# Optimization experiments

Measured on AMD Instinct MI355X. Metric: run time of the kernel, lower is better.

Reference implementation:

```python
import jax, jax.numpy as jnp
import numpy as np

B, N, T, D, DG, DS, NC = 16, 64, 256, 64, 64, 9, 2

def _pe(times, d, max_len):
    # PositionalEncodingTF: timescales = max_len ** linspace(0,1,d//2)
    ts = jnp.asarray(max_len ** np.linspace(0.0, 1.0, d // 2), jnp.float32)
    st = times[..., None] / ts
    return jnp.concatenate([jnp.sin(st), jnp.cos(st)], -1)

def _ln(h, g, b):
    m = h.mean(-1, keepdims=True)
    v = ((h - m) ** 2).mean(-1, keepdims=True)
    return (h - m) * jax.lax.rsqrt(v + 1e-5) * g + b

def setup_inputs():
    key = jax.random.key(0)
    ks = jax.random.split(key, 40)
    s = 0.02
    value = jax.random.normal(ks[0], (B, T, N))
    obs = (jax.random.uniform(ks[1], (B, T, N)) < 0.5).astype(jnp.float32)
    times = jnp.sort(jax.random.uniform(ks[2], (B, T)) * T, axis=1)
    F = D + 2 * DG  # per-node GRU input feature size [x_t, h, time_enc]
    return dict(
        x=jnp.concatenate([value, obs, times[..., None]], -1),
        nufft=jax.random.normal(ks[3], (B, 2, T, N)),
        delta_t=jax.random.uniform(ks[4], (B, T)) * 0.1,
        static=jax.random.normal(ks[5], (B, DS)),
        lengths=jax.random.randint(ks[6], (B,), 1, T + 1),
        proj_w=jax.random.normal(ks[7], (2, D)) * s, proj_b=jnp.zeros(D),
        Wqkv=jax.random.normal(ks[8], (D, 3 * D)) * s, bqkv=jnp.zeros(3 * D),
        Wo=jax.random.normal(ks[9], (D, D)) * s, bo=jnp.zeros(D),
        ln1_g=jnp.ones(D), ln1_b=jnp.zeros(D),
        W1=jax.random.normal(ks[10], (D, D)) * s, b1=jnp.zeros(D),
        W2=jax.random.normal(ks[11], (D, D)) * s, b2=jnp.zeros(D),
        ln2_g=jnp.ones(D), ln2_b=jnp.zeros(D),
        WQ_f=jax.random.normal(ks[12], (T, T)) * 0.05,
        WK_f=jax.random.normal(ks[13], (T, T)) * 0.05,
        Wz=jax.random.normal(ks[14], (2 * F, DG)) * s, bz=jnp.zeros(DG),
        Wr=jax.random.normal(ks[15], (2 * F, DG)) * s, br=jnp.zeros(DG),
        Wc=jax.random.normal(ks[16], (2 * F, DG)) * s, bc=jnp.zeros(DG),
        Wfin=jax.random.normal(ks[17], (DG,)) * s, bfin=jnp.zeros(()),
        We=jax.random.normal(ks[18], (DS, N)) * s, be=jnp.zeros(N),
        Wc1=jax.random.normal(ks[19], (2 * N, 200)) * s, bc1=jnp.zeros(200),
        Wc2=jax.random.normal(ks[20], (200, NC)) * s, bc2=jnp.zeros(NC),
    )

def _forward(x, nufft, delta_t, static, lengths, proj_w, proj_b, Wqkv, bqkv, Wo, bo,
             ln1_g, ln1_b, W1, b1, W2, b2, ln2_g, ln2_b, WQ_f, WK_f,
             Wz, bz, Wr, br, Wc, bc, Wfin, bfin, We, be, Wc1, bc1, Wc2, bc2):
    lengths = jnp.maximum(lengths, 1)
    value = x[:, :, :N].transpose(0, 2, 1)          # (B,N,T)
    obs = x[:, :, N:2 * N].transpose(0, 2, 1)       # (B,N,T) observation mask
    times = x[:, :, -1]                              # (B,T)
    # Conv2d(2->D, 1x1) input projection == per-element linear over [value, mask]
    feat = jnp.stack([value, obs], -1) @ proj_w + proj_b   # (B,N,T,D)
    pe1 = _pe(times, D, T)                           # (B,T,D)
    tin = feat + pe1[:, None]                        # (B,N,T,D)
    # single-head transformer encoder layer (post-norm, relu FFN, eval: no dropout)
    qkv = tin @ Wqkv + bqkv
    q, k, v = jnp.split(qkv, 3, -1)
    scores = jnp.einsum('bnqd,bnkd->bnqk', q, k) / jnp.sqrt(jnp.float32(D))
    kpad = jnp.arange(T)[None, :] >= lengths[:, None]      # (B,T) key padding
    scores = jnp.where(kpad[:, None, None, :], -1e9, scores)
    attn = jax.nn.softmax(scores, -1)
    ao = jnp.einsum('bnqk,bnkd->bnqd', attn, v) @ Wo + bo
    h1 = _ln(tin + ao, ln1_g, ln1_b)
    ff = jax.nn.relu(h1 @ W1 + b1) @ W2 + b2
    tout = _ln(h1 + ff, ln2_g, ln2_b)
    m = obs[..., None]
    x_tat = m * tin + (1.0 - m) * tout               # masked blend (B,N,T,D)
    # Variable_Attention_layer on nufft channel 1: relu-score softmax attention
    xf = nufft[:, 1].transpose(0, 2, 1)              # (B,N,T)
    S = jax.nn.relu(jnp.einsum('bnt,bmt->bnm', xf @ WQ_f, xf @ WK_f)) / jnp.sqrt(jnp.float32(T))
    A = jax.nn.softmax(S, -1).mean(0)                # (N,N)
    A = 0.5 * (A + A.T)
    sm = jax.nn.softmax(A, -1)
    A = 0.5 * (sm + sm.T)
    pe2 = _pe(times, DG, T)                          # (B,T,DG)
    # graph-conv GRU over time (CGRNN) with delta_t decay + length masking
    def stepf(h, inputs):
        xt, tet, dtt, t = inputs                     # (B,N,D),(B,DG),(B,),()
        h = h * jnp.exp(-jax.nn.relu(dtt))[:, None, None]
        te = jnp.broadcast_to(tet[:, None, :], (h.shape[0], N, DG))
        inp = jnp.concatenate([xt, h, te], -1)
        gin = jnp.concatenate([inp, jnp.einsum('nm,bmf->bnf', A, inp)], -1)
        z = jax.nn.sigmoid(gin @ Wz + bz)
        r = jax.nn.sigmoid(gin @ Wr + br)
        inc = jnp.concatenate([xt, r * h, te], -1)
        cin = jnp.concatenate([inc, jnp.einsum('nm,bmf->bnf', A, inc)], -1)
        c = jnp.tanh(cin @ Wc + bc)
        hn = z * h + (1.0 - z) * c
        h = jnp.where((t < lengths)[:, None, None], hn, h)
        return h, None
    h0 = jnp.zeros((x.shape[0], N, DG), x.dtype)
    xs = (x_tat.transpose(2, 0, 1, 3), pe2.transpose(1, 0, 2), delta_t.T, jnp.arange(T))
    hT, _ = jax.lax.scan(stepf, h0, xs)
    out = hT @ Wfin + bfin                           # final 1x1 conv -> (B,N)
    emb = static @ We + be                           # (B,N)
    hcl = jax.nn.relu(jnp.concatenate([out, emb], -1) @ Wc1 + bc1)
    return hcl @ Wc2 + bc2                           # (B,NC)

def reference(x, nufft, delta_t, static, lengths, proj_w, proj_b, Wqkv, bqkv, Wo, bo,
              ln1_g, ln1_b, W1, b1, W2, b2, ln2_g, ln2_b, WQ_f, WK_f,
              Wz, bz, Wr, br, Wc, bc, Wfin, bfin, We, be, Wc1, bc1, Wc2, bc2):
    return _forward(x, nufft, delta_t, static, lengths, proj_w, proj_b, Wqkv, bqkv, Wo, bo,
                    ln1_g, ln1_b, W1, b1, W2, b2, ln2_g, ln2_b, WQ_f, WK_f,
                    Wz, bz, Wr, br, Wc, bc, Wfin, bfin, We, be, Wc1, bc1, Wc2, bc2)
```

## Files before the change

kernel.cpp:

```cpp
#include <hip/hip_runtime.h>
#include <hip/hip_bf16.h>
#include <cmath>

#define DEV __device__ __forceinline__

typedef short s16x8 __attribute__((ext_vector_type(8)));
typedef short s16x4 __attribute__((ext_vector_type(4)));
typedef float f32x4 __attribute__((ext_vector_type(4)));
typedef int   i32x2 __attribute__((ext_vector_type(2)));

DEV unsigned short f2bu(float x){
  __hip_bfloat16 h = __float2bfloat16(x);
  return *reinterpret_cast<unsigned short*>(&h);
}
DEV float bs2f(unsigned short v){ return __uint_as_float(((unsigned)v)<<16); }
DEV float bs2f(short v){ return bs2f((unsigned short)v); }

DEV unsigned cvtpk(float lo, float hi){
  unsigned r;
  asm("v_cvt_pk_bf16_f32 %0, %1, %2" : "=v"(r) : "v"(lo), "v"(hi));
  return r;
}
DEV float dppx1(float v){
  int r = __builtin_amdgcn_mov_dpp(__float_as_int(v), 0xB1, 0xF, 0xF, true);
  return __int_as_float(r);
}

#define BAR() do { asm volatile("s_waitcnt lgkmcnt(0)" ::: "memory"); \
                   __builtin_amdgcn_s_barrier(); \
                   __builtin_amdgcn_sched_barrier(0); } while(0)

DEV int swzo(int row, int col){
  return (row*128 + ((col*2) ^ ((row&7)<<4))) >> 1;
}
DEV s16x8 ldfrag(const short* tile, int t16, int lane, int kk){
  int row = t16 + (lane & 15);
  int c0  = (kk<<5) + ((lane>>4)<<3);
  int off = (row*128 + ((c0<<1) ^ ((row&7)<<4))) >> 1;
  return *(const s16x8*)(tile + off);
}
DEV int swzv(int d, int t){
  return (d*512 + ((t*2) ^ ((d&7)<<4))) >> 1;
}

__global__ void k0_prep(const float* __restrict__ Wqkv, const float* __restrict__ Wo,
                        const float* __restrict__ W1, const float* __restrict__ W2,
                        const float* __restrict__ Wz, const float* __restrict__ Wr,
                        const float* __restrict__ Wc,
                        short* __restrict__ Wqkv_t, short* __restrict__ Wo_t,
                        short* __restrict__ W1_t, short* __restrict__ W2_t,
                        short* __restrict__ Wg_t, short* __restrict__ Wg_h)
{
  int t = blockIdx.x*256 + threadIdx.x;
  if (t < 12288){ int nn=t>>6, k=t&63; Wqkv_t[t]=(short)f2bu(Wqkv[k*192+nn]); }
  else if (t < 16384){ int e=t-12288; int nn=e>>6,k=e&63; Wo_t[e]=(short)f2bu(Wo[k*64+nn]); }
  else if (t < 20480){ int e=t-16384; int nn=e>>6,k=e&63; W1_t[e]=(short)f2bu(W1[k*64+nn]); }
  else if (t < 24576){ int e=t-20480; int nn=e>>6,k=e&63; W2_t[e]=(short)f2bu(W2[k*64+nn]); }
  else if (t < 49152){
    int e=t-24576;
    int g=e>>13, rem=e&8191, s=rem>>12, rem2=rem&4095, c=rem2>>6, k=rem2&63;
    const float* Wg = (g==0)?Wz:((g==1)?Wr:Wc);
    Wg_t[e] = (short)f2bu(Wg[((s?192:0)+k)*64 + c]);
  }
  else if (t < 73728){
    int e=t-49152;
    int g=e>>13, rem=e&8191, s=rem>>12, rem2=rem&4095, c=rem2>>6, k=rem2&63;
    const float* Wg = (g==0)?Wz:((g==1)?Wr:Wc);
    Wg_h[e] = (short)f2bu(Wg[((s?256:64)+k)*64 + c]);
  }
}

__global__ void k1_pe_u(const float* __restrict__ x, const float* __restrict__ delta_t,
                        const float* __restrict__ Wz, const float* __restrict__ bz,
                        const float* __restrict__ Wr, const float* __restrict__ br,
                        const float* __restrict__ Wc, const float* __restrict__ bc,
                        float* __restrict__ pe, float* __restrict__ U, float* __restrict__ decay)
{
  const int q  = threadIdx.x >> 6;
  const int d  = threadIdx.x & 63;
  const int bt = blockIdx.x*4 + q;
  __shared__ float pes[4][64];
  float tmv = x[(size_t)bt*129 + 128];
  int j = d & 31;
  float ts = exp2f((float)j * (8.0f/31.0f));
  float st = tmv / ts;
  float v = (d < 32) ? sinf(st) : cosf(st);
  pes[q][d] = v;
  pe[(size_t)bt*64 + d] = v;
  __syncthreads();
  float a0=bz[d], a1=0.f, a2=br[d], a3=0.f, a4=bc[d], a5=0.f;
  for (int k=0;k<64;k++){
    float p = pes[q][k];
    a0 = fmaf(p, Wz[(128+k)*64+d], a0);
    a1 = fmaf(p, Wz[(320+k)*64+d], a1);
    a2 = fmaf(p, Wr[(128+k)*64+d], a2);
    a3 = fmaf(p, Wr[(320+k)*64+d], a3);
    a4 = fmaf(p, Wc[(128+k)*64+d], a4);
    a5 = fmaf(p, Wc[(320+k)*64+d], a5);
  }
  float* u = U + (size_t)bt*384;
  u[d]=a0; u[64+d]=a1; u[128+d]=a2; u[192+d]=a3; u[256+d]=a4; u[320+d]=a5;
  if (d==0) decay[bt] = expf(-fmaxf(delta_t[bt], 0.f));
}

__global__ void k2a_qfkf(const float* __restrict__ nufft, const float* __restrict__ WQf,
                         const float* __restrict__ WKf, float* __restrict__ qf, float* __restrict__ kf)
{
  const int bn = blockIdx.x, b = bn>>6, n = bn&63;
  const int u = threadIdx.x;
  __shared__ float xs[256];
  xs[u] = nufft[ ((((size_t)b*2)+1)*256 + u)*64 + n ];
  __syncthreads();
  float aq=0.f, ak=0.f;
  for (int t=0;t<256;t++){
    float xv = xs[t];
    aq = fmaf(xv, WQf[t*256+u], aq);
    ak = fmaf(xv, WKf[t*256+u], ak);
  }
  qf[(size_t)bn*256+u]=aq;
  kf[(size_t)bn*256+u]=ak;
}

__launch_bounds__(256, 1)
__global__ void k2b_soft(const float* __restrict__ qf, const float* __restrict__ kf,
                         float* __restrict__ soft)
{
  const int b = blockIdx.x, tid = threadIdx.x;
  __shared__ float qs[64*257];
  __shared__ float ksh[64*257];
  __shared__ float Ss[64*65];
  const float* qb = qf + ((size_t)b<<14);
  const float* kb = kf + ((size_t)b<<14);
  for (int e=tid; e<16384; e+=256){
    int r=e>>8, c=e&255;
    qs[r*257+c]=qb[e];
    ksh[r*257+c]=kb[e];
  }
  __syncthreads();
  const int n = tid>>2, m0 = (tid&3)<<4;
  float acc[16];
  #pragma unroll
  for (int i=0;i<16;i++) acc[i]=0.f;
  for (int t=0;t<256;t++){
    float qv = qs[n*257+t];
    #pragma unroll
    for (int i=0;i<16;i++) acc[i] = fmaf(qv, ksh[(m0+i)*257+t], acc[i]);
  }
  #pragma unroll
  for (int i=0;i<16;i++) Ss[n*65+m0+i] = fmaxf(acc[i],0.f)*(1.f/16.f);
  __syncthreads();
  if (tid < 64){
    float mx=-1e30f;
    for (int m=0;m<64;m++) mx=fmaxf(mx, Ss[tid*65+m]);
    float s=0.f;
    for (int m=0;m<64;m++) s += expf(Ss[tid*65+m]-mx);
    float inv=1.f/s;
    for (int m=0;m<64;m++) soft[((size_t)b<<12)+(tid<<6)+m] = expf(Ss[tid*65+m]-mx)*inv;
  }
}

__global__ void k2c_A(const float* __restrict__ soft, short* __restrict__ Abf,
                      float* __restrict__ rs_out)
{
  const int tid = threadIdx.x;
  __shared__ float A0[64*65];
  __shared__ float A1[64*65];
  for (int e=tid; e<4096; e+=256){
    int nn=e>>6, mm=e&63;
    float s=0.f;
    #pragma unroll
    for (int b=0;b<16;b++) s += soft[((size_t)b<<12)+e];
    A0[nn*65+mm] = s*(1.f/16.f);
  }
  __syncthreads();
  for (int e=tid; e<4096; e+=256){
    int nn=e>>6, mm=e&63;
    A1[nn*65+mm] = 0.5f*(A0[nn*65+mm]+A0[mm*65+nn]);
  }
  __syncthreads();
  if (tid < 64){
    float mx=-1e30f;
    for (int m=0;m<64;m++) mx=fmaxf(mx, A1[tid*65+m]);
    float s=0.f;
    for (int m=0;m<64;m++) s += expf(A1[tid*65+m]-mx);
    float inv=1.f/s;
    for (int m=0;m<64;m++) A0[tid*65+m] = expf(A1[tid*65+m]-mx)*inv;
  }
  __syncthreads();
  for (int e=tid; e<4096; e+=256){
    int nn=e>>6, mm=e&63;
    float a = 0.5f*(A0[nn*65+mm]+A0[mm*65+nn]);
    A1[nn*65+mm] = a;
    Abf[e] = (short)f2bu(a);
  }
  __syncthreads();
  if (tid < 64){
    float s=0.f;
    for (int m=0;m<64;m++) s += A1[tid*65+m];
    rs_out[tid]=s;
  }
}

__launch_bounds__(512, 1)
__global__ void k3_former(const float* __restrict__ x, const float* __restrict__ pe_g,
    const float* __restrict__ proj_w, const float* __restrict__ proj_b,
    const short* __restrict__ Wqkv_t, const float* __restrict__ bqkv,
    const short* __restrict__ Wo_t, const float* __restrict__ bo,
    const float* __restrict__ ln1g, const float* __restrict__ ln1b,
    const short* __restrict__ W1_t, const float* __restrict__ b1,
    const short* __restrict__ W2_t, const float* __restrict__ b2,
    const float* __restrict__ ln2g, const float* __restrict__ ln2b,
    const int* __restrict__ lengths, unsigned short* __restrict__ xtat)
{
  const int bn = blockIdx.x, b = bn>>6, n = bn&63;
  const int tid = threadIdx.x, w = tid>>6, lane = tid&63;
  const int l15 = lane&15, lhi = lane>>4;
  __shared__ short tp_s[16384];
  __shared__ short q_s[16384];
  __shared__ short k_s[16384];
  __shared__ short v_t[16384];
  __shared__ float valr[256], obsr[256];

  int len = lengths[b]; if (len<1) len=1;
  const int LT = (len+15)>>4;
  const int KB = (len+63)>>6;

  if (tid < 256){
    const float* xr = x + ((size_t)b*256+tid)*129;
    valr[tid]=xr[n]; obsr[tid]=xr[64+n];
  }
  for (int e=tid; e<16384; e+=512) v_t[e]=0;
  __syncthreads();

  const int nrows = LT<<4;
  for (int e=tid; e<(nrows<<6); e+=512){
    int t=e>>6, d=e&63;
    float ti = fmaf(valr[t],proj_w[d], fmaf(obsr[t],proj_w[64+d], proj_b[d]))
             + pe_g[(((size_t)b<<8)+t)*64+d];
    tp_s[swzo(t,d)] = (short)f2bu(ti);
  }
  __syncthreads();

  #pragma unroll
  for (int j=0;j<2;j++){
    const int rt = w + (j<<3);
    if (rt < LT){
      s16x8 a0 = ldfrag(tp_s, rt<<4, lane, 0);
      s16x8 a1 = ldfrag(tp_s, rt<<4, lane, 1);
      const int rb = (rt<<4) + (lhi<<2);
      #pragma unroll
      for (int nt=0; nt<12; nt++){
        const short* wb = Wqkv_t + (((nt<<4)+l15)<<6) + (lhi<<3);
        s16x8 b0 = *(const s16x8*)wb;
        s16x8 b1v = *(const s16x8*)(wb+32);
        float bias = bqkv[(nt<<4)+l15];
        f32x4 acc = {bias,bias,bias,bias};
        acc = __builtin_amdgcn_mfma_f32_16x16x32_bf16(a0,b0,acc,0,0,0);
        acc = __builtin_amdgcn_mfma_f32_16x16x32_bf16(a1,b1v,acc,0,0,0);
        const int col = ((nt&3)<<4) + l15;
        if (nt<4){
          #pragma unroll
          for(int i=0;i<4;i++) q_s[swzo(rb+i,col)] = (short)f2bu(acc[i]*0.125f);
        } else if (nt<8){
          #pragma unroll
          for(int i=0;i<4;i++) k_s[swzo(rb+i,col)] = (short)f2bu(acc[i]);
        } else {
          #pragma unroll
          for(int i=0;i<4;i++) v_t[swzv(col, rb+i)] = (short)f2bu(acc[i]);
        }
      }
    }
  }
  __syncthreads();

  f32x4 Oac[2][4];
  float rsum[2][4];
  #pragma unroll
  for(int j=0;j<2;j++)
    #pragma unroll
    for(int dt=0;dt<4;dt++) Oac[j][dt]=(f32x4){0.f,0.f,0.f,0.f};
  #pragma unroll
  for(int j=0;j<2;j++)
    #pragma unroll
    for(int i=0;i<4;i++) rsum[j][i]=0.f;

  for (int kb=0; kb<KB; kb++){
    s16x8 kf[4][2];
    #pragma unroll
    for (int ct=0;ct<4;ct++){
      kf[ct][0]=ldfrag(k_s, (((kb<<2)+ct)<<4), lane, 0);
      kf[ct][1]=ldfrag(k_s, (((kb<<2)+ct)<<4), lane, 1);
    }
    #pragma unroll
    for (int j=0;j<2;j++){
      const int rt=w+(j<<3);
      if (rt < LT){
        s16x8 q0=ldfrag(q_s, rt<<4, lane, 0);
        s16x8 q1=ldfrag(q_s, rt<<4, lane, 1);
        const int rb=(rt<<4)+(lhi<<2);
        #pragma unroll
        for (int ct=0;ct<4;ct++){
          f32x4 s={0.f,0.f,0.f,0.f};
          s=__builtin_amdgcn_mfma_f32_16x16x32_bf16(q0,kf[ct][0],s,0,0,0);
          s=__builtin_amdgcn_mfma_f32_16x16x32_bf16(q1,kf[ct][1],s,0,0,0);
          const int key=(kb<<6)+(ct<<4)+l15;
          #pragma unroll
          for(int i=0;i<4;i++){
            float p = (key<len) ? __expf(s[i]) : 0.f;
            rsum[j][i]+=p;
            tp_s[swzo(rb+i,(ct<<4)+l15)] = (short)f2bu(p);
          }
        }
      }
    }
    __syncthreads();
    s16x8 vf[4][2];
    #pragma unroll
    for (int dt=0;dt<4;dt++){
      const int d=(dt<<4)+l15;
      #pragma unroll
      for (int kk=0;kk<2;kk++){
        const int k0=(kk<<5)+(lhi<<3);
        vf[dt][kk] = *(const s16x8*)(v_t + swzv(d, (kb<<6)+k0));
      }
    }
    #pragma unroll
    for (int j=0;j<2;j++){
      const int rt=w+(j<<3);
      if (rt < LT){
        s16x8 p0=ldfrag(tp_s, rt<<4, lane, 0);
        s16x8 p1=ldfrag(tp_s, rt<<4, lane, 1);
        #pragma unroll
        for (int dt=0;dt<4;dt++){
          Oac[j][dt]=__builtin_amdgcn_mfma_f32_16x16x32_bf16(p0,vf[dt][0],Oac[j][dt],0,0,0);
          Oac[j][dt]=__builtin_amdgcn_mfma_f32_16x16x32_bf16(p1,vf[dt][1],Oac[j][dt],0,0,0);
        }
      }
    }
    __syncthreads();
  }

  float inv[2][4];
  #pragma unroll
  for(int j=0;j<2;j++)
    #pragma unroll
    for(int i=0;i<4;i++){
      float v=rsum[j][i];
      v += __shfl_xor(v,1); v += __shfl_xor(v,2); v += __shfl_xor(v,4); v += __shfl_xor(v,8);
      inv[j][i]=1.f/v;
    }

  #pragma unroll
  for (int j=0;j<2;j++){
    const int rt=w+(j<<3);
    if (rt < LT){
      const int rb=(rt<<4)+(lhi<<2);
      #pragma unroll
      for (int dt=0;dt<4;dt++)
        #pragma unroll
        for (int i=0;i<4;i++)
          q_s[swzo(rb+i,(dt<<4)+l15)] = (short)f2bu(Oac[j][dt][i]*inv[j][i]);
    }
  }
  __syncthreads();

  f32x4 h1[2][4];
  #pragma unroll
  for (int j=0;j<2;j++){
    const int rt=w+(j<<3);
    if (rt < LT){
      s16x8 a0=ldfrag(q_s, rt<<4, lane, 0);
      s16x8 a1=ldfrag(q_s, rt<<4, lane, 1);
      const int rb=(rt<<4)+(lhi<<2);
      #pragma unroll
      for (int dt=0;dt<4;dt++){
        const int col=(dt<<4)+l15;
        const short* wb = Wo_t + (col<<6) + (lhi<<3);
        s16x8 b0=*(const s16x8*)wb, b1v=*(const s16x8*)(wb+32);
        float bias=bo[col];
        f32x4 acc={bias,bias,bias,bias};
        acc=__builtin_amdgcn_mfma_f32_16x16x32_bf16(a0,b0,acc,0,0,0);
        acc=__builtin_amdgcn_mfma_f32_16x16x32_bf16(a1,b1v,acc,0,0,0);
        #pragma unroll
        for(int i=0;i<4;i++){
          const int row=rb+i;
          acc[i]+= fmaf(valr[row],proj_w[col], fmaf(obsr[row],proj_w[64+col], proj_b[col]))
                 + pe_g[(((size_t)b<<8)+row)*64+col];
        }
        h1[j][dt]=acc;
      }
      f32x4 mu, rsq;
      #pragma unroll
      for(int i=0;i<4;i++){
        float sv = h1[j][0][i]+h1[j][1][i]+h1[j][2][i]+h1[j][3][i];
        sv += __shfl_xor(sv,1); sv+=__shfl_xor(sv,2); sv+=__shfl_xor(sv,4); sv+=__shfl_xor(sv,8);
        mu[i]=sv*(1.f/64.f);
      }
      #pragma unroll
      for(int i=0;i<4;i++){
        float sv=0.f;
        #pragma unroll
        for(int dt=0;dt<4;dt++){ float c=h1[j][dt][i]-mu[i]; sv=fmaf(c,c,sv); }
        sv += __shfl_xor(sv,1); sv+=__shfl_xor(sv,2); sv+=__shfl_xor(sv,4); sv+=__shfl_xor(sv,8);
        rsq[i]=1.f/sqrtf(sv*(1.f/64.f)+1e-5f);
      }
      #pragma unroll
      for(int dt=0;dt<4;dt++){
        const int col=(dt<<4)+l15;
        float g=ln1g[col], bb=ln1b[col];
        #pragma unroll
        for(int i=0;i<4;i++){
          float hv=(h1[j][dt][i]-mu[i])*rsq[i]*g+bb;
          h1[j][dt][i]=hv;
          k_s[swzo(rb+i,col)] = (short)f2bu(hv);
        }
      }
    }
  }
  __syncthreads();

  #pragma unroll
  for (int j=0;j<2;j++){
    const int rt=w+(j<<3);
    if (rt < LT){
      s16x8 a0=ldfrag(k_s, rt<<4, lane, 0);
      s16x8 a1=ldfrag(k_s, rt<<4, lane, 1);
      const int rb=(rt<<4)+(lhi<<2);
      #pragma unroll
      for (int dt=0;dt<4;dt++){
        const int col=(dt<<4)+l15;
        const short* wb = W1_t + (col<<6)+(lhi<<3);
        s16x8 b0=*(const s16x8*)wb, b1v=*(const s16x8*)(wb+32);
        float bias=b1[col];
        f32x4 acc={bias,bias,bias,bias};
        acc=__builtin_amdgcn_mfma_f32_16x16x32_bf16(a0,b0,acc,0,0,0);
        acc=__builtin_amdgcn_mfma_f32_16x16x32_bf16(a1,b1v,acc,0,0,0);
        #pragma unroll
        for(int i=0;i<4;i++) tp_s[swzo(rb+i,col)]=(short)f2bu(fmaxf(acc[i],0.f));
      }
    }
  }
  __syncthreads();

  #pragma unroll
  for (int j=0;j<2;j++){
    const int rt=w+(j<<3);
    if (rt < LT){
      s16x8 a0=ldfrag(tp_s, rt<<4, lane, 0);
      s16x8 a1=ldfrag(tp_s, rt<<4, lane, 1);
      const int rb=(rt<<4)+(lhi<<2);
      f32x4 to[4];
      #pragma unroll
      for (int dt=0;dt<4;dt++){
        const int col=(dt<<4)+l15;
        const short* wb = W2_t + (col<<6)+(lhi<<3);
        s16x8 b0=*(const s16x8*)wb, b1v=*(const s16x8*)(wb+32);
        float bias=b2[col];
        f32x4 acc={bias,bias,bias,bias};
        acc=__builtin_amdgcn_mfma_f32_16x16x32_bf16(a0,b0,acc,0,0,0);
        acc=__builtin_amdgcn_mfma_f32_16x16x32_bf16(a1,b1v,acc,0,0,0);
        acc += h1[j][dt];
        to[dt]=acc;
      }
      f32x4 mu, rsq;
      #pragma unroll
      for(int i=0;i<4;i++){
        float sv = to[0][i]+to[1][i]+to[2][i]+to[3][i];
        sv += __shfl_xor(sv,1); sv+=__shfl_xor(sv,2); sv+=__shfl_xor(sv,4); sv+=__shfl_xor(sv,8);
        mu[i]=sv*(1.f/64.f);
      }
      #pragma unroll
      for(int i=0;i<4;i++){
        float sv=0.f;
        #pragma unroll
        for(int dt=0;dt<4;dt++){ float c=to[dt][i]-mu[i]; sv=fmaf(c,c,sv); }
        sv += __shfl_xor(sv,1); sv+=__shfl_xor(sv,2); sv+=__shfl_xor(sv,4); sv+=__shfl_xor(sv,8);
        rsq[i]=1.f/sqrtf(sv*(1.f/64.f)+1e-5f);
      }
      #pragma unroll
      for(int dt=0;dt<4;dt++){
        const int col=(dt<<4)+l15;
        float g=ln2g[col], bb=ln2b[col];
        #pragma unroll
        for(int i=0;i<4;i++){
          const int row=rb+i;
          if (row < len){
            float tv=(to[dt][i]-mu[i])*rsq[i]*g+bb;
            float tin = fmaf(valr[row],proj_w[col], fmaf(obsr[row],proj_w[64+col], proj_b[col]))
                      + pe_g[(((size_t)b<<8)+row)*64+col];
            float ob = obsr[row];
            xtat[((size_t)bn<<14)+(row<<6)+col] = f2bu(ob*tin + (1.f-ob)*tv);
          }
        }
      }
    }
  }
}

__global__ void k35_xg(const unsigned short* __restrict__ xtat, const short* __restrict__ Abf,
                       const short* __restrict__ Wg_t, const int* __restrict__ lengths,
                       const float* __restrict__ U, const float* __restrict__ rs_g,
                       unsigned short* __restrict__ Xall)
{
  const int bt = blockIdx.x, b = bt>>8, t = bt&255;
  int len = lengths[b]; if (len<1) len=1;
  if (t >= len) return;
  const int tid = threadIdx.x, w = tid>>6, lane = tid&63;
  const int l15 = lane&15, lhi = lane>>4;
  __shared__ short xt_rm[4096], xt_tp[4096], axt_rm[4096];

  #pragma unroll
  for (int q=0;q<2;q++){
    int e = tid + (q<<8);
    int nn = e>>3, c0 = (e&7)<<3;
    s16x8 v = *(const s16x8*)((const short*)xtat + (((size_t)(b*64+nn)*256 + t)<<6) + c0);
    *(s16x8*)(xt_rm + swzo(nn,c0)) = v;
    #pragma unroll
    for (int jj=0;jj<8;jj++) xt_tp[swzo(c0+jj, nn)] = v[jj];
  }
  __syncthreads();

  {
    s16x8 bx[2];
    #pragma unroll
    for (int kk=0;kk<2;kk++) bx[kk]=ldfrag(xt_tp, w<<4, lane, kk);
    #pragma unroll
    for (int rt=0;rt<4;rt++){
      f32x4 acc={0.f,0.f,0.f,0.f};
      #pragma unroll
      for (int kk=0;kk<2;kk++){
        s16x8 af = *(const s16x8*)(Abf + ((rt<<4)+l15)*64 + (kk<<5) + (lhi<<3));
        acc=__builtin_amdgcn_mfma_f32_16x16x32_bf16(af,bx[kk],acc,0,0,0);
      }
      const int rb=(rt<<4)+(lhi<<2);
      #pragma unroll
      for(int i=0;i<4;i++) axt_rm[swzo(rb+i,(w<<4)+l15)] = (short)f2bu(acc[i]);
    }
  }
  __syncthreads();

  s16x8 fx[4][2], fa[4][2];
  #pragma unroll
  for (int rt=0;rt<4;rt++)
    #pragma unroll
    for (int kk=0;kk<2;kk++){
      fx[rt][kk]=ldfrag(xt_rm, rt<<4, lane, kk);
      fa[rt][kk]=ldfrag(axt_rm, rt<<4, lane, kk);
    }
  const int dcol = (w<<4)+l15;
  f32x4 rsv[4];
  #pragma unroll
  for (int rt=0;rt<4;rt++) rsv[rt] = *(const f32x4*)(rs_g + (rt<<4) + (lhi<<2));
  const float* Ub = U + (size_t)bt*384;
  #pragma unroll
  for (int g=0; g<3; g++){
    s16x8 wbx[2], wba[2];
    #pragma unroll
    for (int kk=0;kk<2;kk++){
      wbx[kk] = *(const s16x8*)(Wg_t + (((g<<1)  )*64 + dcol)*64 + (kk<<5)+(lhi<<3));
      wba[kk] = *(const s16x8*)(Wg_t + (((g<<1)+1)*64 + dcol)*64 + (kk<<5)+(lhi<<3));
    }
    float u1 = Ub[(g<<7) + dcol];
    float u2 = Ub[(g<<7) + 64 + dcol];
    #pragma unroll
    for (int rt=0;rt<4;rt++){
      f32x4 acc={u1,u1,u1,u1};
      #pragma unroll
      for (int kk=0;kk<2;kk++){
        acc=__builtin_amdgcn_mfma_f32_16x16x32_bf16(fx[rt][kk],wbx[kk],acc,0,0,0);
        acc=__builtin_amdgcn_mfma_f32_16x16x32_bf16(fa[rt][kk],wba[kk],acc,0,0,0);
      }
      s16x4 pk;
      #pragma unroll
      for(int i=0;i<4;i++) pk[i]=(short)f2bu(acc[i] + rsv[rt][i]*u2);
      *(s16x4*)((short*)Xall + (((size_t)bt*3 + g)*64 + dcol)*64 + (rt<<4)+(lhi<<2)) = pk;
    }
  }
}

__launch_bounds__(512, 1)
__global__ void k4_scan(const unsigned short* __restrict__ Xall,
                        const float* __restrict__ decay, const short* __restrict__ Abf,
                        const short* __restrict__ Wg_h,
                        const int* __restrict__ lengths, float* __restrict__ hT)
{
  const int b = blockIdx.x, tid = threadIdx.x;
  const int w = tid>>6, lane = tid&63;
  const int l15 = lane&15, lhi = lane>>4;
  const int pe_ = l15&1;
  const int rnt = w>>1, dp = w&1;
  const int nb_ = (rnt<<4) + (lhi<<2);
  const int d0 = (dp<<5) + l15, d1 = (dp<<5) + 16 + l15;
  const int tmA0 = (w&1)<<1, tmA1 = tmA0+1;
  const int dnA = w>>1;

  __shared__ short h_rm[4096], h_tp[4096], ah_rm[4096];
  __shared__ short rh_rm[4096], rh_tp[4096], arh_rm[4096];
  __shared__ float dec_s[256];

  int len = lengths[b]; if (len<1) len=1;
  for (int e=tid; e<256; e+=512) dec_s[e] = decay[b*256+e];

  s16x8 aA[2][2];
  #pragma unroll
  for (int t2=0;t2<2;t2++)
    #pragma unroll
    for (int kk=0;kk<2;kk++)
      aA[t2][kk] = *(const s16x8*)(Abf + (((t2?tmA1:tmA0)<<4) + l15)*64 + (kk<<5) + (lhi<<3));

  s16x8 wf[3][2][2][2];
  #pragma unroll
  for (int g=0;g<3;g++)
    #pragma unroll
    for (int s=0;s<2;s++)
      #pragma unroll
      for (int kk=0;kk<2;kk++)
        #pragma unroll
        for (int e=0;e<2;e++)
          wf[g][s][kk][e] = *(const s16x8*)(Wg_h + (((g*2+s)*64 + (e?d1:d0))<<6) + (kk<<5) + (lhi<<3));

  int tpo[2];
  #pragma unroll
  for (int e=0;e<2;e++){ int r = e?d1:d0; tpo[e] = r*128 + (((nb_)*2) ^ ((r&7)<<4)); }
  int rmo[4];
  { int dPr = ((dp<<1) + pe_)*16 + (l15 & ~1);
    #pragma unroll
    for (int i=0;i<4;i++){ int n = nb_+i; rmo[i] = n*128 + ((dPr*2) ^ ((n&7)<<4)); } }
  int amo[4];
  { int dAr = (dnA<<4) + (l15 & ~1);
    int tb = (pe_? tmA1 : tmA0)<<4;
    #pragma unroll
    for (int i=0;i<4;i++){ int n = tb + (lhi<<2) + i; amo[i] = n*128 + ((dAr*2) ^ ((n&7)<<4)); } }
  int rdT[2], rdR[2];
  { int r = (dnA<<4)+l15;
    #pragma unroll
    for (int kk=0;kk<2;kk++) rdT[kk] = r*128 + (((kk<<6) + (lhi<<4)) ^ ((r&7)<<4)); }
  { int r = (rnt<<4)+l15;
    #pragma unroll
    for (int kk=0;kk<2;kk++) rdR[kk] = r*128 + (((kk<<6) + (lhi<<4)) ^ ((r&7)<<4)); }

  f32x4 hreg[2] = {{0.f,0.f,0.f,0.f},{0.f,0.f,0.f,0.f}};
  f32x4 zz[2];

  const short* Xb = (const short*)Xall;
  s16x4 xzc[2], xrc[2], xcc[2], xzn[2], xrn[2], xcn[2];
  #pragma unroll
  for (int e=0;e<2;e++){ xzc[e]=(s16x4){0,0,0,0}; xrc[e]=xzc[e]; xcc[e]=xzc[e]; }
  {
    const short* base = Xb + ((size_t)(b*256))*12288;
    #pragma unroll
    for (int e=0;e<2;e++){
      int de = e?d1:d0;
      xzc[e] = *(const s16x4*)(base + (0*64 + de)*64 + nb_);
      xrc[e] = *(const s16x4*)(base + (1*64 + de)*64 + nb_);
      xcc[e] = *(const s16x4*)(base + (2*64 + de)*64 + nb_);
    }
  }
  __syncthreads();

  for (int t=0; t<len; t++){
    float dc = dec_s[t];
    #pragma unroll
    for (int e=0;e<2;e++)
      #pragma unroll
      for (int i=0;i<4;i++) hreg[e][i] *= dc;

    #pragma unroll
    for (int e=0;e<2;e++){ xzn[e]=(s16x4){0,0,0,0}; xrn[e]=xzn[e]; xcn[e]=xzn[e]; }
    if (t+1 < len){
      const short* base = Xb + ((size_t)(b*256 + t+1))*12288;
      #pragma unroll
      for (int e=0;e<2;e++){
        int de = e?d1:d0;
        xzn[e] = *(const s16x4*)(base + (0*64 + de)*64 + nb_);
        xrn[e] = *(const s16x4*)(base + (1*64 + de)*64 + nb_);
        xcn[e] = *(const s16x4*)(base + (2*64 + de)*64 + nb_);
      }
    }

    #pragma unroll
    for (int e=0;e<2;e++){
      i32x2 v; v[0] = (int)cvtpk(hreg[e][0], hreg[e][1]);
               v[1] = (int)cvtpk(hreg[e][2], hreg[e][3]);
      *(i32x2*)((char*)h_tp + tpo[e]) = v;
    }
    #pragma unroll
    for (int i=0;i<4;i++){
      float v0 = hreg[0][i], v1 = hreg[1][i];
      float n0 = dppx1(v0), n1 = dppx1(v1);
      float lo = pe_ ? n1 : v0;
      float hi = pe_ ? v1 : n0;
      *(unsigned*)((char*)h_rm + rmo[i]) = cvtpk(lo, hi);
    }
    BAR();

    {
      s16x8 bh0 = *(const s16x8*)((const char*)h_tp + rdT[0]);
      s16x8 bh1 = *(const s16x8*)((const char*)h_tp + rdT[1]);
      f32x4 a0v={0.f,0.f,0.f,0.f}, a1v={0.f,0.f,0.f,0.f};
      a0v = __builtin_amdgcn_mfma_f32_16x16x32_bf16(aA[0][0], bh0, a0v, 0,0,0);
      a0v = __builtin_amdgcn_mfma_f32_16x16x32_bf16(aA[0][1], bh1, a0v, 0,0,0);
      a1v = __builtin_amdgcn_mfma_f32_16x16x32_bf16(aA[1][0], bh0, a1v, 0,0,0);
      a1v = __builtin_amdgcn_mfma_f32_16x16x32_bf16(aA[1][1], bh1, a1v, 0,0,0);
      #pragma unroll
      for (int i=0;i<4;i++){
        float n0 = dppx1(a0v[i]), n1 = dppx1(a1v[i]);
        float lo = pe_ ? n1 : a0v[i];
        float hi = pe_ ? a1v[i] : n0;
        *(unsigned*)((char*)ah_rm + amo[i]) = cvtpk(lo, hi);
      }
    }
    BAR();

    {
      s16x8 fh0 = *(const s16x8*)((const char*)h_rm  + rdR[0]);
      s16x8 fh1 = *(const s16x8*)((const char*)h_rm  + rdR[1]);
      s16x8 fa0 = *(const s16x8*)((const char*)ah_rm + rdR[0]);
      s16x8 fa1 = *(const s16x8*)((const char*)ah_rm + rdR[1]);
      f32x4 gz[2], gr[2], rh[2];
      #pragma unroll
      for (int e=0;e<2;e++)
        #pragma unroll
        for (int i=0;i<4;i++){ gz[e][i]=bs2f(xzc[e][i]); gr[e][i]=bs2f(xrc[e][i]); }
      #pragma unroll
      for (int e=0;e<2;e++){
        gz[e] = __builtin_amdgcn_mfma_f32_16x16x32_bf16(fh0, wf[0][0][0][e], gz[e], 0,0,0);
        gz[e] = __builtin_amdgcn_mfma_f32_16x16x32_bf16(fh1, wf[0][0][1][e], gz[e], 0,0,0);
        gz[e] = __builtin_amdgcn_mfma_f32_16x16x32_bf16(fa0, wf[0][1][0][e], gz[e], 0,0,0);
        gz[e] = __builtin_amdgcn_mfma_f32_16x16x32_bf16(fa1, wf[0][1][1][e], gz[e], 0,0,0);
        gr[e] = __builtin_amdgcn_mfma_f32_16x16x32_bf16(fh0, wf[1][0][0][e], gr[e], 0,0,0);
        gr[e] = __builtin_amdgcn_mfma_f32_16x16x32_bf16(fh1, wf[1][0][1][e], gr[e], 0,0,0);
        gr[e] = __builtin_amdgcn_mfma_f32_16x16x32_bf16(fa0, wf[1][1][0][e], gr[e], 0,0,0);
        gr[e] = __builtin_amdgcn_mfma_f32_16x16x32_bf16(fa1, wf[1][1][1][e], gr[e], 0,0,0);
      }
      #pragma unroll
      for (int e=0;e<2;e++)
        #pragma unroll
        for (int i=0;i<4;i++){
          float zv = 1.f/(1.f+__expf(-gz[e][i]));
          float rv = 1.f/(1.f+__expf(-gr[e][i]));
          zz[e][i] = zv;
          rh[e][i] = rv * hreg[e][i];
        }
      #pragma unroll
      for (int e=0;e<2;e++){
        i32x2 v; v[0] = (int)cvtpk(rh[e][0], rh[e][1]);
                 v[1] = (int)cvtpk(rh[e][2], rh[e][3]);
        *(i32x2*)((char*)rh_tp + tpo[e]) = v;
      }
      #pragma unroll
      for (int i=0;i<4;i++){
        float v0 = rh[0][i], v1 = rh[1][i];
        float n0 = dppx1(v0), n1 = dppx1(v1);
        float lo = pe_ ? n1 : v0;
        float hi = pe_ ? v1 : n0;
        *(unsigned*)((char*)rh_rm + rmo[i]) = cvtpk(lo, hi);
      }
    }
    BAR();

    {
      s16x8 br0 = *(const s16x8*)((const char*)rh_tp + rdT[0]);
      s16x8 br1 = *(const s16x8*)((const char*)rh_tp + rdT[1]);
      f32x4 a0v={0.f,0.f,0.f,0.f}, a1v={0.f,0.f,0.f,0.f};
      a0v = __builtin_amdgcn_mfma_f32_16x16x32_bf16(aA[0][0], br0, a0v, 0,0,0);
      a0v = __builtin_amdgcn_mfma_f32_16x16x32_bf16(aA[0][1], br1, a0v, 0,0,0);
      a1v = __builtin_amdgcn_mfma_f32_16x16x32_bf16(aA[1][0], br0, a1v, 0,0,0);
      a1v = __builtin_amdgcn_mfma_f32_16x16x32_bf16(aA[1][1], br1, a1v, 0,0,0);
      #pragma unroll
      for (int i=0;i<4;i++){
        float n0 = dppx1(a0v[i]), n1 = dppx1(a1v[i]);
        float lo = pe_ ? n1 : a0v[i];
        float hi = pe_ ? a1v[i] : n0;
        *(unsigned*)((char*)arh_rm + amo[i]) = cvtpk(lo, hi);
      }
    }
    BAR();

    {
      s16x8 fr0 = *(const s16x8*)((const char*)rh_rm  + rdR[0]);
      s16x8 fr1 = *(const s16x8*)((const char*)rh_rm  + rdR[1]);
      s16x8 fb0 = *(const s16x8*)((const char*)arh_rm + rdR[0]);
      s16x8 fb1 = *(const s16x8*)((const char*)arh_rm + rdR[1]);
      f32x4 gc[2];
      #pragma unroll
      for (int e=0;e<2;e++)
        #pragma unroll
        for (int i=0;i<4;i++) gc[e][i]=bs2f(xcc[e][i]);
      #pragma unroll
      for (int e=0;e<2;e++){
        gc[e] = __builtin_amdgcn_mfma_f32_16x16x32_bf16(fr0, wf[2][0][0][e], gc[e], 0,0,0);
        gc[e] = __builtin_amdgcn_mfma_f32_16x16x32_bf16(fr1, wf[2][0][1][e], gc[e], 0,0,0);
        gc[e] = __builtin_amdgcn_mfma_f32_16x16x32_bf16(fb0, wf[2][1][0][e], gc[e], 0,0,0);
        gc[e] = __builtin_amdgcn_mfma_f32_16x16x32_bf16(fb1, wf[2][1][1][e], gc[e], 0,0,0);
      }
      #pragma unroll
      for (int e=0;e<2;e++)
        #pragma unroll
        for (int i=0;i<4;i++){
          float cv = 1.f - 2.f/(__expf(2.f*gc[e][i])+1.f);
          hreg[e][i] = fmaf(zz[e][i], hreg[e][i]-cv, cv);
        }
    }

    #pragma unroll
    for (int e=0;e<2;e++){ xzc[e]=xzn[e]; xrc[e]=xrn[e]; xcc[e]=xcn[e]; }
  }

  float sp = 1.f;
  for (int t=len; t<256; t++) sp *= dec_s[t];
  #pragma unroll
  for (int e=0;e<2;e++)
    #pragma unroll
    for (int i=0;i<4;i++)
      hT[(((size_t)b<<6) + nb_ + i)*64 + (e?d1:d0)] = hreg[e][i]*sp;
}

__global__ void k5_head(const float* __restrict__ hT, const float* __restrict__ Wfin,
                        const float* __restrict__ bfin,
                        const float* __restrict__ stat, const float* __restrict__ We,
                        const float* __restrict__ be,
                        const float* __restrict__ Wc1, const float* __restrict__ bc1,
                        const float* __restrict__ Wc2, const float* __restrict__ bc2,
                        float* __restrict__ out)
{
  const int b = blockIdx.x, tid = threadIdx.x;
  __shared__ float cat[128];
  __shared__ float hcl[200];
  if (tid < 64){
    const float* hr = hT + (((size_t)b<<6)+tid)*64;
    float a = bfin[0];
    #pragma unroll
    for (int d=0;d<64;d++) a = fmaf(hr[d], Wfin[d], a);
    cat[tid]=a;
  } else if (tid < 128){
    int nn = tid-64;
    float a = be[nn];
    #pragma unroll
    for (int k=0;k<9;k++) a = fmaf(stat[b*9+k], We[k*64+nn], a);
    cat[tid]=a;
  }
  __syncthreads();
  if (tid < 200){
    float a = bc1[tid];
    for (int k=0;k<128;k++) a = fmaf(cat[k], Wc1[k*200+tid], a);
    hcl[tid] = fmaxf(a, 0.f);
  }
  __syncthreads();
  if (tid < 2){
    float a = bc2[tid];
    for (int k=0;k<200;k++) a = fmaf(hcl[k], Wc2[k*2+tid], a);
    out[b*2+tid] = a;
  }
}

extern "C" void kernel_launch(void* const* d_in, const int* in_sizes, int n_in,
                              void* d_out, int out_size, void* d_ws, size_t ws_size,
                              hipStream_t stream)
{
  const float* x       = (const float*)d_in[0];
  const float* nufft   = (const float*)d_in[1];
  const float* delta_t = (const float*)d_in[2];
  const float* stat    = (const float*)d_in[3];
  const int*   lengths = (const int*)  d_in[4];
  const float* proj_w  = (const float*)d_in[5];
  const float* proj_b  = (const float*)d_in[6];
  const float* Wqkv    = (const float*)d_in[7];
  const float* bqkv    = (const float*)d_in[8];
  const float* Wo      = (const float*)d_in[9];
  const float* bo      = (const float*)d_in[10];
  const float* ln1g    = (const float*)d_in[11];
  const float* ln1b    = (const float*)d_in[12];
  const float* W1      = (const float*)d_in[13];
  const float* b1      = (const float*)d_in[14];
  const float* W2      = (const float*)d_in[15];
  const float* b2      = (const float*)d_in[16];
  const float* ln2g    = (const float*)d_in[17];
  const float* ln2b    = (const float*)d_in[18];
  const float* WQf     = (const float*)d_in[19];
  const float* WKf     = (const float*)d_in[20];
  const float* Wz      = (const float*)d_in[21];
  const float* bz      = (const float*)d_in[22];
  const float* Wr      = (const float*)d_in[23];
  const float* br      = (const float*)d_in[24];
  const float* Wc      = (const float*)d_in[25];
  const float* bc      = (const float*)d_in[26];
  const float* Wfin    = (const float*)d_in[27];
  const float* bfin    = (const float*)d_in[28];
  const float* We      = (const float*)d_in[29];
  const float* be      = (const float*)d_in[30];
  const float* Wc1     = (const float*)d_in[31];
  const float* bc1     = (const float*)d_in[32];
  const float* Wc2     = (const float*)d_in[33];
  const float* bc2     = (const float*)d_in[34];
  float* out = (float*)d_out;

  char* ws = (char*)d_ws;
  size_t o = 0;
  float* pe    = (float*)(ws+o); o += (size_t)4096*64*4;
  float* U     = (float*)(ws+o); o += (size_t)4096*384*4;
  float* decay = (float*)(ws+o); o += (size_t)4096*4;
  unsigned short* xtat = (unsigned short*)(ws+o); o += (size_t)1024*256*64*2;
  float* qf    = (float*)(ws+o); o += (size_t)1024*256*4;
  float* kf    = (float*)(ws+o); o += (size_t)1024*256*4;
  float* soft  = (float*)(ws+o); o += (size_t)16*4096*4;
  short* Abf   = (short*)(ws+o); o += (size_t)4096*2;
  float* rs    = (float*)(ws+o); o += (size_t)64*4;
  float* hT    = (float*)(ws+o); o += (size_t)16*64*64*4;
  short* Wqkv_t= (short*)(ws+o); o += (size_t)12288*2;
  short* Wo_t  = (short*)(ws+o); o += (size_t)4096*2;
  short* W1_t  = (short*)(ws+o); o += (size_t)4096*2;
  short* W2_t  = (short*)(ws+o); o += (size_t)4096*2;
  short* Wg_t  = (short*)(ws+o); o += (size_t)24576*2;
  short* Wg_h  = (short*)(ws+o); o += (size_t)24576*2;
  unsigned short* Xall = (unsigned short*)(ws+o); o += (size_t)4096*3*4096*2;
  (void)ws_size; (void)in_sizes; (void)n_in; (void)out_size;

  hipLaunchKernelGGL(k0_prep,   dim3(288),  dim3(256), 0, stream,
                     Wqkv, Wo, W1, W2, Wz, Wr, Wc, Wqkv_t, Wo_t, W1_t, W2_t, Wg_t, Wg_h);
  hipLaunchKernelGGL(k1_pe_u,   dim3(1024), dim3(256), 0, stream,
                     x, delta_t, Wz, bz, Wr, br, Wc, bc, pe, U, decay);
  hipLaunchKernelGGL(k2a_qfkf,  dim3(1024), dim3(256), 0, stream,
                     nufft, WQf, WKf, qf, kf);
  hipLaunchKernelGGL(k2b_soft,  dim3(16),   dim3(256), 0, stream, qf, kf, soft);
  hipLaunchKernelGGL(k2c_A,     dim3(1),    dim3(256), 0, stream, soft, Abf, rs);
  hipLaunchKernelGGL(k3_former, dim3(1024), dim3(512), 0, stream,
                     x, pe, proj_w, proj_b, Wqkv_t, bqkv, Wo_t, bo, ln1g, ln1b,
                     W1_t, b1, W2_t, b2, ln2g, ln2b, lengths, xtat);
  hipLaunchKernelGGL(k35_xg,    dim3(4096), dim3(256), 0, stream,
                     xtat, Abf, Wg_t, lengths, U, rs, Xall);
  hipLaunchKernelGGL(k4_scan,   dim3(16),   dim3(512), 0, stream,
                     Xall, decay, Abf, Wg_h, lengths, hT);
  hipLaunchKernelGGL(k5_head,   dim3(16),   dim3(256), 0, stream,
                     hT, Wfin, bfin, stat, We, be, Wc1, bc1, Wc2, bc2, out);
}
```

Baseline: 865.1 us.

## Pack two batch scans per 1024-thread block in GRU scan kernel

The recurrent scan kernel now runs two batch elements per block (two 512-thread groups with separate shared-memory slices), launching 8 blocks instead of 16. The loop runs to the larger of the two lengths, and the shorter group masks its updates. The apparent intent is to interleave two independent serial recurrences on one compute unit to hide latency, at the cost of half as many CUs in use, lockstep barriers between groups, and wasted work when the lengths differ. The register budget per thread also shrinks under the 1024-thread launch bound.

```diff
diff --git a/kernel.cpp b/kernel.cpp
--- a/kernel.cpp
+++ b/kernel.cpp
@@ -578,28 +578,35 @@
   }
 }
 
-__launch_bounds__(512, 1)
+__launch_bounds__(1024, 1)
 __global__ void k4_scan(const unsigned short* __restrict__ Xall,
                         const float* __restrict__ decay, const short* __restrict__ Abf,
                         const short* __restrict__ Wg_h,
                         const int* __restrict__ lengths, float* __restrict__ hT)
 {
-  const int b = blockIdx.x, tid = threadIdx.x;
-  const int w = tid>>6, lane = tid&63;
+  const int tid = threadIdx.x;
+  const int grp = tid >> 9;
+  const int stid = tid & 511;
+  const int w = stid>>6, lane = stid&63;
   const int l15 = lane&15, lhi = lane>>4;
   const int pe_ = l15&1;
+  const int b = blockIdx.x*2 + grp;
+  const int gofs = grp << 13;
   const int rnt = w>>1, dp = w&1;
   const int nb_ = (rnt<<4) + (lhi<<2);
   const int d0 = (dp<<5) + l15, d1 = (dp<<5) + 16 + l15;
   const int tmA0 = (w&1)<<1, tmA1 = tmA0+1;
   const int dnA = w>>1;
 
-  __shared__ short h_rm[4096], h_tp[4096], ah_rm[4096];
-  __shared__ short rh_rm[4096], rh_tp[4096], arh_rm[4096];
-  __shared__ float dec_s[256];
-
-  int len = lengths[b]; if (len<1) len=1;
-  for (int e=tid; e<256; e+=512) dec_s[e] = decay[b*256+e];
+  __shared__ short h_rm[2][4096], h_tp[2][4096], ah_rm[2][4096];
+  __shared__ short rh_rm[2][4096], rh_tp[2][4096], arh_rm[2][4096];
+  __shared__ float dec_s[2][256];
+
+  int lenA = lengths[blockIdx.x*2];   if (lenA<1) lenA=1;
+  int lenB = lengths[blockIdx.x*2+1]; if (lenB<1) lenB=1;
+  const int len = grp ? lenB : lenA;
+  const int lenmax = (lenA>lenB)?lenA:lenB;
+  for (int e=stid; e<256; e+=512) dec_s[grp][e] = decay[b*256+e];
 
   s16x8 aA[2][2];
   #pragma unroll
@@ -621,23 +628,23 @@
 
   int tpo[2];
   #pragma unroll
-  for (int e=0;e<2;e++){ int r = e?d1:d0; tpo[e] = r*128 + (((nb_)*2) ^ ((r&7)<<4)); }
+  for (int e=0;e<2;e++){ int r = e?d1:d0; tpo[e] = gofs + r*128 + (((nb_)*2) ^ ((r&7)<<4)); }
   int rmo[4];
   { int dPr = ((dp<<1) + pe_)*16 + (l15 & ~1);
     #pragma unroll
-    for (int i=0;i<4;i++){ int n = nb_+i; rmo[i] = n*128 + ((dPr*2) ^ ((n&7)<<4)); } }
+    for (int i=0;i<4;i++){ int n = nb_+i; rmo[i] = gofs + n*128 + ((dPr*2) ^ ((n&7)<<4)); } }
   int amo[4];
   { int dAr = (dnA<<4) + (l15 & ~1);
     int tb = (pe_? tmA1 : tmA0)<<4;
     #pragma unroll
-    for (int i=0;i<4;i++){ int n = tb + (lhi<<2) + i; amo[i] = n*128 + ((dAr*2) ^ ((n&7)<<4)); } }
+    for (int i=0;i<4;i++){ int n = tb + (lhi<<2) + i; amo[i] = gofs + n*128 + ((dAr*2) ^ ((n&7)<<4)); } }
   int rdT[2], rdR[2];
   { int r = (dnA<<4)+l15;
     #pragma unroll
-    for (int kk=0;kk<2;kk++) rdT[kk] = r*128 + (((kk<<6) + (lhi<<4)) ^ ((r&7)<<4)); }
+    for (int kk=0;kk<2;kk++) rdT[kk] = gofs + r*128 + (((kk<<6) + (lhi<<4)) ^ ((r&7)<<4)); }
   { int r = (rnt<<4)+l15;
     #pragma unroll
-    for (int kk=0;kk<2;kk++) rdR[kk] = r*128 + (((kk<<6) + (lhi<<4)) ^ ((r&7)<<4)); }
+    for (int kk=0;kk<2;kk++) rdR[kk] = gofs + r*128 + (((kk<<6) + (lhi<<4)) ^ ((r&7)<<4)); }
 
   f32x4 hreg[2] = {{0.f,0.f,0.f,0.f},{0.f,0.f,0.f,0.f}};
   f32x4 zz[2];
@@ -658,8 +665,9 @@
   }
   __syncthreads();
 
-  for (int t=0; t<len; t++){
-    float dc = dec_s[t];
+  for (int t=0; t<lenmax; t++){
+    const bool act = (t < len);
+    float dc = act ? dec_s[grp][t] : 1.f;
     #pragma unroll
     for (int e=0;e<2;e++)
       #pragma unroll
@@ -794,13 +802,15 @@
         gc[e] = __builtin_amdgcn_mfma_f32_16x16x32_bf16(fb0, wf[2][1][0][e], gc[e], 0,0,0);
         gc[e] = __builtin_amdgcn_mfma_f32_16x16x32_bf16(fb1, wf[2][1][1][e], gc[e], 0,0,0);
       }
-      #pragma unroll
-      for (int e=0;e<2;e++)
-        #pragma unroll
-        for (int i=0;i<4;i++){
-          float cv = 1.f - 2.f/(__expf(2.f*gc[e][i])+1.f);
-          hreg[e][i] = fmaf(zz[e][i], hreg[e][i]-cv, cv);
-        }
+      if (act){
+        #pragma unroll
+        for (int e=0;e<2;e++)
+          #pragma unroll
+          for (int i=0;i<4;i++){
+            float cv = 1.f - 2.f/(__expf(2.f*gc[e][i])+1.f);
+            hreg[e][i] = fmaf(zz[e][i], hreg[e][i]-cv, cv);
+          }
+      }
     }
 
     #pragma unroll
@@ -808,7 +818,7 @@
   }
 
   float sp = 1.f;
-  for (int t=len; t<256; t++) sp *= dec_s[t];
+  for (int t=len; t<256; t++) sp *= dec_s[grp][t];
   #pragma unroll
   for (int e=0;e<2;e++)
     #pragma unroll
@@ -929,7 +939,7 @@
                      W1_t, b1, W2_t, b2, ln2g, ln2b, lengths, xtat);
   hipLaunchKernelGGL(k35_xg,    dim3(4096), dim3(256), 0, stream,
                      xtat, Abf, Wg_t, lengths, U, rs, Xall);
-  hipLaunchKernelGGL(k4_scan,   dim3(16),   dim3(512), 0, stream,
+  hipLaunchKernelGGL(k4_scan,   dim3(8),    dim3(1024), 0, stream,
                      Xall, decay, Abf, Wg_h, lengths, hT);
   hipLaunchKernelGGL(k5_head,   dim3(16),   dim3(256), 0, stream,
                      hT, Wfin, bfin, stat, We, be, Wc1, bc1, Wc2, bc2, out);
```

After: 2.864 ms. 3.31x slower.
